# Kernel optimization log

Measured on AMD Instinct MI355X. Metric: run time of the kernel, lower is better.

Reference implementation:

```python
import jax, jax.numpy as jnp
import numpy as np

PRECS = 1e-05
# HBV parameter scaling bounds (order: BETA, FC, K0, K1, K2, LP, PERC, UZL, TT, CFMAX, CFR, CWH, BETAET)
LB = jnp.array([1.0, 50.0, 0.05, 0.01, 0.001, 0.2, 0.0, 0.0, -2.5, 0.5, 0.0, 0.0, 0.3], dtype=jnp.float32)
UB = jnp.array([6.0, 1000.0, 0.9, 0.5, 0.2, 1.0, 10.0, 100.0, 2.5, 10.0, 0.1, 0.2, 5.0], dtype=jnp.float32)

NSTEP, NGRID, MU = 730, 1000, 8

def setup_inputs() -> dict:
    key = jax.random.key(0)
    k1, k2, k3, k4 = jax.random.split(key, 4)
    P = jax.random.uniform(k1, (NSTEP, NGRID), jnp.float32) * 10.0      # precip mm/day
    T = jax.random.normal(k2, (NSTEP, NGRID), jnp.float32) * 8.0 + 2.0  # temp degC
    ET = jax.random.uniform(k3, (NSTEP, NGRID), jnp.float32) * 5.0      # PET mm/day
    x = jnp.stack([P, T, ET], axis=-1)                                   # [Nstep, Ngrid, 3]
    parameters = jax.random.uniform(k4, (NSTEP, NGRID, 13, MU), jnp.float32)  # raw in [0,1]
    tdlst = jnp.arange(2, dtype=jnp.int32)  # -> param indices {12, 0} = BETAET, BETA dynamic
    return {"x": x, "parameters": parameters, "staind": NSTEP - 1, "tdlst": tdlst, "mu": MU}

def _hbv_forward(x, parameters, staind, tdlst):
    # scale raw params to physical ranges: [Nstep, Ngrid, 13, mu]
    parT = LB[None, None, :, None] + parameters * (UB - LB)[None, None, :, None]
    # static params taken from time index staind, broadcast over time
    parhbv = jnp.broadcast_to(parT[staind][None], parT.shape)
    # dynamic params: dydrop=0 -> bernoulli mask is all zeros -> comPar = dynPar
    idx = jnp.mod(jnp.asarray(tdlst) - 1, 13)
    parhbv = parhbv.at[:, :, idx, :].set(parT[:, :, idx, :])

    Ngrid = x.shape[1]
    mu = parameters.shape[-1]
    init = tuple(jnp.full((Ngrid, mu), 0.001, dtype=jnp.float32) for _ in range(5))

    def step(carry, inp):
        SP, MW, SM, SUZ, SLZ = carry
        P_, T_, ET_, par = inp              # P_/T_/ET_: [Ngrid], par: [Ngrid, 13, mu]
        P_, T_, ET_ = P_[:, None], T_[:, None], ET_[:, None]
        BETA, FC, K0, K1, K2, LP, PERCc, UZL, TT, CFMAX, CFR, CWH, BETAET = (
            par[:, i] for i in range(13))
        is_rain = (T_ >= TT).astype(jnp.float32)
        RAIN = P_ * is_rain
        SNOW = P_ * (1.0 - is_rain)
        SP = SP + SNOW
        melt = jnp.minimum(jnp.maximum(CFMAX * (T_ - TT), 0.0), SP)
        MW = MW + melt
        SP = SP - melt
        refr = jnp.minimum(jnp.maximum(CFR * CFMAX * (TT - T_), 0.0), MW)
        SP = SP + refr
        MW = MW - refr
        tosoil = jnp.maximum(MW - CWH * SP, 0.0)
        MW = MW - tosoil
        soil_wetness = jnp.clip((SM / FC) ** BETA, 0.0, 1.0)
        recharge = (RAIN + tosoil) * soil_wetness
        SM = SM + RAIN + tosoil - recharge
        excess = jnp.maximum(SM - FC, 0.0)
        SM = SM - excess
        evapfactor = jnp.clip((SM / (LP * FC)) ** BETAET, 0.0, 1.0)
        ETact = jnp.minimum(SM, ET_ * evapfactor)
        SM = jnp.maximum(SM - ETact, PRECS)
        SUZ = SUZ + recharge + excess
        PERC = jnp.minimum(SUZ, PERCc)
        SUZ = SUZ - PERC
        Q0 = K0 * jnp.maximum(SUZ - UZL, 0.0)
        SUZ = SUZ - Q0
        Q1 = K1 * SUZ
        SUZ = SUZ - Q1
        SLZ = SLZ + PERC
        Q2 = K2 * SLZ
        SLZ = SLZ - Q2
        return (SP, MW, SM, SUZ, SLZ), Q0 + Q1 + Q2

    _, Qsimmu = jax.lax.scan(step, init, (x[:, :, 0], x[:, :, 1], x[:, :, 2], parhbv))
    # muwts=None -> mean over components; routOpt=False -> Qs = Qsimave[..., None]
    return Qsimmu.mean(-1)[..., None]  # [Nstep, Ngrid, 1]

def reference(x, parameters, staind, tdlst, mu):
    return _hbv_forward(x, parameters, staind, tdlst)
```

## Files before the change

kernel.cpp:

```cpp
#include <hip/hip_runtime.h>

#define NSTEP 730
#define NGRID 1000
#define MU    8
#define NPAR  13
#define PRECS 1e-5f

#define PAR_TSTRIDE 104000u
#define PAR_GSTRIDE 104u
#define X_TSTRIDE 3000u

#define GSTEPS 10
#define NGROUP (NSTEP / GSTEPS)

#define G5  5
#define NG5 (NSTEP / G5)

constexpr float LB_[NPAR] = {1.0f, 50.0f, 0.05f, 0.01f, 0.001f, 0.2f, 0.0f,
                             0.0f, -2.5f, 0.5f, 0.0f, 0.0f, 0.3f};
constexpr float UB_[NPAR] = {6.0f, 1000.0f, 0.9f, 0.5f, 0.2f, 1.0f, 10.0f,
                             100.0f, 2.5f, 10.0f, 0.1f, 0.2f, 5.0f};

__device__ __forceinline__ float fast_rcp(float x)  { return __builtin_amdgcn_rcpf(x); }
__device__ __forceinline__ float fast_exp2(float x) { return __builtin_amdgcn_exp2f(x); }
__device__ __forceinline__ float fast_log2(float x) { return __builtin_amdgcn_logf(x); }

__device__ __forceinline__ int mod13(int v) {
    int r = v % NPAR;
    if (r < 0) r += NPAR;
    return r;
}

template <int CTRL>
__device__ __forceinline__ float dpp_xadd(float v) {
    int r = __builtin_amdgcn_update_dpp(0, __float_as_int(v), CTRL, 0xF, 0xF, true);
    return v + __int_as_float(r);
}
__device__ __forceinline__ float mu8_sum(float v) {
    v = dpp_xadd<0xB1>(v);
    v = dpp_xadd<0x4E>(v);
    int s = __builtin_amdgcn_ds_swizzle(__float_as_int(v), 0x101F);
    return v + __int_as_float(s);
}

__device__ __forceinline__ void hbv_fast_12_0(
    const float* __restrict__ x, const float* __restrict__ par,
    int staind, float* __restrict__ out, int g, int m)
{
    const unsigned cpar = (unsigned)g * PAR_GSTRIDE + (unsigned)m;
    const unsigned g3   = (unsigned)g * 3u;

    float fx[NPAR];
    const unsigned sbase = (unsigned)staind * PAR_TSTRIDE + cpar;
#pragma unroll
    for (int i = 0; i < NPAR; ++i)
        fx[i] = fmaf(par[sbase + (unsigned)i * 8u], UB_[i] - LB_[i], LB_[i]);
    const float FC = fx[1], K0 = fx[2], K1 = fx[3], K2 = fx[4], LP = fx[5],
                PERCc = fx[6], UZL = fx[7], TT = fx[8], CFMAX = fx[9],
                CFR = fx[10], CWH = fx[11];
    const float rcpFC    = fast_rcp(FC);
    const float rcpLPFC  = fast_rcp(LP * FC);
    const float l2rcpFC  = fast_log2(rcpFC);
    const float l2rcpLPF = fast_log2(rcpLPFC);
    const float CC       = CFR * CFMAX;
    constexpr float lbB = LB_[0],  dvB = UB_[0]  - LB_[0];
    constexpr float lbE = LB_[12], dvE = UB_[12] - LB_[12];

    float bP[3][G5], bT[3][G5], bE[3][G5], b0[3][G5], b1[3][G5];
    float SP = 0.001f, MW = 0.001f, SM = 0.001f, SUZ = 0.001f, SLZ = 0.001f;

    auto load = [&](int b, int t0) {
#pragma unroll
        for (int j = 0; j < G5; ++j) {
            unsigned t  = (unsigned)(t0 + j);
            unsigned xo = t * X_TSTRIDE + g3;
            bP[b][j] = x[xo];
            bT[b][j] = x[xo + 1u];
            bE[b][j] = x[xo + 2u];
            unsigned po = t * PAR_TSTRIDE + cpar;
            b0[b][j] = par[po + 96u];
            b1[b][j] = par[po + 0u];
        }
    };

    auto compute = [&](int b, int t0) {
        float RAINv[G5], SNOWv[G5], MAXCM[G5], MAXRF[G5], ETv[G5];
        float BETAv[G5], BETEv[G5], bbc[G5], ebc[G5];
#pragma unroll
        for (int j = 0; j < G5; ++j) {
            float Pj = bP[b][j], Tj = bT[b][j];
            float dT = Tj - TT;
            float RAIN = (dT >= 0.f) ? Pj : 0.f;
            RAINv[j] = RAIN;
            SNOWv[j] = Pj - RAIN;
            float cm = CFMAX * dT;
            MAXCM[j] = fmaxf(cm, 0.f);
            MAXRF[j] = fmaxf(-CC * dT, 0.f);
            ETv[j]   = bE[b][j];
            float BETAET = fmaf(b0[b][j], dvE, lbE);
            float BETA   = fmaf(b1[b][j], dvB, lbB);
            BETAv[j] = BETA;  BETEv[j] = BETAET;
            bbc[j] = BETA   * l2rcpFC;
            ebc[j] = BETAET * l2rcpLPF;
        }
        float ql[G5];
#pragma unroll
        for (int j = 0; j < G5; ++j) {
            SP += SNOWv[j];
            float melt = fminf(MAXCM[j], SP);
            MW += melt; SP -= melt;
            float refr = fminf(MAXRF[j], MW);
            SP += refr; MW -= refr;
            float tosoil = fmaxf(fmaf(-CWH, SP, MW), 0.f);
            MW -= tosoil;
            float rt   = RAINv[j] + tosoil;
            float smrt = SM + rt;
            float soilw = fast_exp2(fmaf(BETAv[j], fast_log2(SM), bbc[j]));
            float rech  = rt * soilw;
            float SM_mid = smrt - rech;
            float SM_ae  = fminf(SM_mid, FC);
            float excess = SM_mid - SM_ae;
            float evapf  = fminf(fast_exp2(fmaf(BETEv[j], fast_log2(SM_ae), ebc[j])), 1.f);
            SM = fmaxf(fmaf(-ETv[j], evapf, SM_ae), PRECS);
            SUZ += rech + excess;
            float PERC = fminf(SUZ, PERCc);
            float SUZp = SUZ - PERC;
            float Q0   = K0 * fmaxf(SUZp - UZL, 0.f);
            float SUZq = SUZp - Q0;
            float Q1   = K1 * SUZq;
            SUZ = SUZq - Q1;
            SLZ += PERC;
            float Q2 = K2 * SLZ;
            SLZ -= Q2;
            ql[j] = (Q0 + Q1) + Q2;
        }
#pragma unroll
        for (int j = 0; j < G5; ++j) ql[j] = mu8_sum(ql[j]);
        if (m == 0) {
#pragma unroll
            for (int j = 0; j < G5; ++j)
                out[(unsigned)(t0 + j) * (unsigned)NGRID + (unsigned)g] = ql[j] * 0.125f;
        }
    };

    load(0, 0);
    load(1, G5);
    int grp = 0;
    for (int it = 0; it < 48; ++it, grp += 3) {
        load(2, (grp + 2) * G5); compute(0, grp * G5);
        load(0, (grp + 3) * G5); compute(1, (grp + 1) * G5);
        load(1, (grp + 4) * G5); compute(2, (grp + 2) * G5);
    }
    compute(0, 144 * G5);
    compute(1, 145 * G5);
}

__device__ __forceinline__ float hbv_step_core(
    float P_, float T_, float ET_,
    float BETA, float FC, float K0, float K1, float K2,
    float PERCc, float UZL, float TT, float CFMAX, float CFR, float CWH,
    float BETAET, float rcpFC, float rcpLPFC,
    float& SP, float& MW, float& SM, float& SUZ, float& SLZ)
{
    float dT    = T_ - TT;
    float RAIN  = (T_ >= TT) ? P_ : 0.f;
    float SNOW  = P_ - RAIN;
    SP += SNOW;
    float cm    = CFMAX * dT;
    float melt  = fminf(fmaxf(cm, 0.f), SP);
    MW += melt; SP -= melt;
    float refr  = fminf(fmaxf(-CFR * cm, 0.f), MW);
    SP += refr; MW -= refr;
    float tosoil = fmaxf(MW - CWH * SP, 0.f);
    MW -= tosoil;
    float soilw  = fminf(fast_exp2(BETA * fast_log2(SM * rcpFC)), 1.f);
    float rt     = RAIN + tosoil;
    float rech   = rt * soilw;
    SM += rt - rech;
    float excess = fmaxf(SM - FC, 0.f);
    SM -= excess;
    float evapf  = fminf(fast_exp2(BETAET * fast_log2(SM * rcpLPFC)), 1.f);
    float ETact  = fminf(SM, ET_ * evapf);
    SM = fmaxf(SM - ETact, PRECS);
    SUZ += rech + excess;
    float PERC = fminf(SUZ, PERCc);
    SUZ -= PERC;
    float Q0 = K0 * fmaxf(SUZ - UZL, 0.f);
    SUZ -= Q0;
    float Q1 = K1 * SUZ;
    SUZ -= Q1;
    SLZ += PERC;
    float Q2 = K2 * SLZ;
    SLZ -= Q2;
    return Q0 + Q1 + Q2;
}

__device__ void hbv_generic2(
    const float* __restrict__ x, const float* __restrict__ par,
    int staind, int idx0, int idx1, float* __restrict__ out, int g, int m)
{
    const unsigned cpar = (unsigned)g * PAR_GSTRIDE + (unsigned)m;
    const unsigned g3   = (unsigned)g * 3u;

    float lb0 = 0.f, dv0 = 0.f, lb1 = 0.f, dv1 = 0.f;
    float sel0[NPAR], sel1[NPAR];
#pragma unroll
    for (int i = 0; i < NPAR; ++i) {
        sel0[i] = (idx0 == i) ? 1.f : 0.f;
        sel1[i] = (idx1 == i && idx1 != idx0) ? 1.f : 0.f;
        if (idx0 == i) { lb0 = LB_[i]; dv0 = UB_[i] - LB_[i]; }
        if (idx1 == i) { lb1 = LB_[i]; dv1 = UB_[i] - LB_[i]; }
    }
    const unsigned off0 = (unsigned)idx0 * 8u, off1 = (unsigned)idx1 * 8u;

    float basep[NPAR];
    const unsigned sbase = (unsigned)staind * PAR_TSTRIDE + cpar;
#pragma unroll
    for (int i = 0; i < NPAR; ++i) {
        float fxv = fmaf(par[sbase + (unsigned)i * 8u], UB_[i] - LB_[i], LB_[i]);
        basep[i] = fxv * (1.f - sel0[i] - sel1[i]);
    }

    float bP[2][GSTEPS], bT[2][GSTEPS], bEv[2][GSTEPS];
    float bS0[2][GSTEPS], bS1[2][GSTEPS];
    float SP = 0.001f, MW = 0.001f, SM = 0.001f, SUZ = 0.001f, SLZ = 0.001f;

    auto load = [&](int b, int t0) {
#pragma unroll
        for (int j = 0; j < GSTEPS; ++j) {
            unsigned t  = (unsigned)(t0 + j);
            unsigned xo = t * X_TSTRIDE + g3;
            bP[b][j]  = x[xo];
            bT[b][j]  = x[xo + 1u];
            bEv[b][j] = x[xo + 2u];
            unsigned po = t * PAR_TSTRIDE + cpar;
            bS0[b][j] = par[po + off0];
            bS1[b][j] = par[po + off1];
        }
    };
    auto compute = [&](int b, int t0) {
        float ql[GSTEPS];
#pragma unroll
        for (int j = 0; j < GSTEPS; ++j) {
            float sv0 = fmaf(bS0[b][j], dv0, lb0);
            float sv1 = fmaf(bS1[b][j], dv1, lb1);
            float pr[NPAR];
#pragma unroll
            for (int i = 0; i < NPAR; ++i)
                pr[i] = fmaf(sel1[i], sv1, fmaf(sel0[i], sv0, basep[i]));
            float rcpFC   = fast_rcp(pr[1]);
            float rcpLPFC = fast_rcp(pr[5] * pr[1]);
            ql[j] = hbv_step_core(bP[b][j], bT[b][j], bEv[b][j],
                                  pr[0], pr[1], pr[2], pr[3], pr[4], pr[6],
                                  pr[7], pr[8], pr[9], pr[10], pr[11], pr[12],
                                  rcpFC, rcpLPFC, SP, MW, SM, SUZ, SLZ);
        }
#pragma unroll
        for (int j = 0; j < GSTEPS; ++j) {
            float s = mu8_sum(ql[j]);
            if (m == 0)
                out[(unsigned)(t0 + j) * (unsigned)NGRID + (unsigned)g] = s * 0.125f;
        }
    };

    load(0, 0);
    for (int gp = 0; gp < NGROUP; gp += 2) {
        if (gp + 1 < NGROUP) load(1, (gp + 1) * GSTEPS);
        compute(0, gp * GSTEPS);
        if (gp + 2 < NGROUP) load(0, (gp + 2) * GSTEPS);
        if (gp + 1 < NGROUP) compute(1, (gp + 1) * GSTEPS);
    }
}

__global__ __launch_bounds__(64, 1) void hbv_main(
    const float* __restrict__ x, const float* __restrict__ par,
    const int* __restrict__ staind_p, const int* __restrict__ tdlst_p,
    float* __restrict__ out)
{
    const int tid = blockIdx.x * 64 + threadIdx.x;
    const int g   = tid >> 3;
    const int m   = tid & 7;

    const int staind = __builtin_amdgcn_readfirstlane(staind_p[0]);
    const int idx0   = __builtin_amdgcn_readfirstlane(mod13(tdlst_p[0] - 1));
    const int idx1   = __builtin_amdgcn_readfirstlane(mod13(tdlst_p[1] - 1));

    if (idx0 == 12 && idx1 == 0)
        hbv_fast_12_0(x, par, staind, out, g, m);
    else
        hbv_generic2(x, par, staind, idx0, idx1, out, g, m);
}

__global__ __launch_bounds__(64, 1) void hbv_scan_generic(
    const float* __restrict__ x, const float* __restrict__ par,
    const int* __restrict__ staind_p, const int* __restrict__ tdlst_p,
    int n_td, float* __restrict__ out)
{
    const int tid = blockIdx.x * 64 + threadIdx.x;
    const int g   = tid >> 3;
    const int m   = tid & 7;
    if (g >= NGRID) return;

    const int staind    = staind_p[0];
    const unsigned cpar = (unsigned)g * PAR_GSTRIDE + (unsigned)m;
    const unsigned g3   = (unsigned)g * 3u;

    unsigned off[NPAR], st[NPAR];
#pragma unroll
    for (int i = 0; i < NPAR; ++i) {
        bool vr = false;
        for (int j = 0; j < n_td; ++j)
            if (mod13(tdlst_p[j] - 1) == i) vr = true;
        off[i] = (vr ? 0u : (unsigned)staind * PAR_TSTRIDE) + cpar + (unsigned)i * 8u;
        st[i]  = vr ? PAR_TSTRIDE : 0u;
    }

    float SP = 0.001f, MW = 0.001f, SM = 0.001f, SUZ = 0.001f, SLZ = 0.001f;
    for (int t = 0; t < NSTEP; ++t) {
        unsigned xo = (unsigned)t * X_TSTRIDE + g3;
        float P_ = x[xo], T_ = x[xo + 1u], E_ = x[xo + 2u];
        float pr[NPAR];
#pragma unroll
        for (int i = 0; i < NPAR; ++i) {
            pr[i] = fmaf(par[off[i]], UB_[i] - LB_[i], LB_[i]);
            off[i] += st[i];
        }
        float rcpFC   = fast_rcp(pr[1]);
        float rcpLPFC = fast_rcp(pr[5] * pr[1]);
        float q = hbv_step_core(P_, T_, E_, pr[0], pr[1], pr[2], pr[3], pr[4],
                                pr[6], pr[7], pr[8], pr[9], pr[10], pr[11],
                                pr[12], rcpFC, rcpLPFC, SP, MW, SM, SUZ, SLZ);
        float s = mu8_sum(q);
        if (m == 0) out[(unsigned)t * (unsigned)NGRID + (unsigned)g] = s * 0.125f;
    }
}

extern "C" void kernel_launch(void* const* d_in, const int* in_sizes, int n_in,
                              void* d_out, int out_size, void* d_ws, size_t ws_size,
                              hipStream_t stream) {
    const float* x      = (const float*)d_in[0];
    const float* par    = (const float*)d_in[1];
    const int*   staind = (const int*)d_in[2];
    const int*   tdlst  = (const int*)d_in[3];
    float*       out    = (float*)d_out;
    const int n_td = in_sizes[3];

    const int threads = NGRID * MU;
    const int block   = 64;
    const int grid    = (threads + block - 1) / block;

    if (n_td == 2)
        hbv_main<<<grid, block, 0, stream>>>(x, par, staind, tdlst, out);
    else
        hbv_scan_generic<<<grid, block, 0, stream>>>(x, par, staind, tdlst,
                                                     n_td, out);
}
```

Baseline: 430.9 us.

## Split HBV scan into producer and consumer waves with LDS double buffering

Each block now holds two waves. A producer wave loads forcing and dynamic parameters three groups ahead, precomputes the per-step terms (rain/snow split, melt limits, exponent constants) into double-buffered LDS, and reduces and writes the outputs. The consumer wave runs only the serial recurrence, reading precomputed inputs from LDS. The aim is to take global-memory latency, the preparation math and the reductions off the serial dependency chain. The cost is a __syncthreads per group of 10 steps plus extra LDS traffic, and the grid is still only 125 blocks.

Result: faster. 420.7 us (-2.4%).

```diff
diff --git a/kernel.cpp b/kernel.cpp
--- a/kernel.cpp
+++ b/kernel.cpp
@@ -2,7 +2,6 @@
 
 #define NSTEP 730
 #define NGRID 1000
-#define MU    8
 #define NPAR  13
 #define PRECS 1e-5f
 
@@ -10,11 +9,16 @@
 #define PAR_GSTRIDE 104u
 #define X_TSTRIDE 3000u
 
+#define G10   10
+#define NG10  73
+
 #define GSTEPS 10
-#define NGROUP (NSTEP / GSTEPS)
-
-#define G5  5
-#define NG5 (NSTEP / G5)
+#define NGROUP 73
+
+#define LDS_PREP_BUF 5760
+#define LDS_QL_BASE  11520
+#define LDS_QL_BUF   640
+#define LDS_TOTAL    12800
 
 constexpr float LB_[NPAR] = {1.0f, 50.0f, 0.05f, 0.01f, 0.001f, 0.2f, 0.0f,
                              0.0f, -2.5f, 0.5f, 0.0f, 0.0f, 0.3f};
@@ -41,118 +45,6 @@
     v = dpp_xadd<0x4E>(v);
     int s = __builtin_amdgcn_ds_swizzle(__float_as_int(v), 0x101F);
     return v + __int_as_float(s);
-}
-
-__device__ __forceinline__ void hbv_fast_12_0(
-    const float* __restrict__ x, const float* __restrict__ par,
-    int staind, float* __restrict__ out, int g, int m)
-{
-    const unsigned cpar = (unsigned)g * PAR_GSTRIDE + (unsigned)m;
-    const unsigned g3   = (unsigned)g * 3u;
-
-    float fx[NPAR];
-    const unsigned sbase = (unsigned)staind * PAR_TSTRIDE + cpar;
-#pragma unroll
-    for (int i = 0; i < NPAR; ++i)
-        fx[i] = fmaf(par[sbase + (unsigned)i * 8u], UB_[i] - LB_[i], LB_[i]);
-    const float FC = fx[1], K0 = fx[2], K1 = fx[3], K2 = fx[4], LP = fx[5],
-                PERCc = fx[6], UZL = fx[7], TT = fx[8], CFMAX = fx[9],
-                CFR = fx[10], CWH = fx[11];
-    const float rcpFC    = fast_rcp(FC);
-    const float rcpLPFC  = fast_rcp(LP * FC);
-    const float l2rcpFC  = fast_log2(rcpFC);
-    const float l2rcpLPF = fast_log2(rcpLPFC);
-    const float CC       = CFR * CFMAX;
-    constexpr float lbB = LB_[0],  dvB = UB_[0]  - LB_[0];
-    constexpr float lbE = LB_[12], dvE = UB_[12] - LB_[12];
-
-    float bP[3][G5], bT[3][G5], bE[3][G5], b0[3][G5], b1[3][G5];
-    float SP = 0.001f, MW = 0.001f, SM = 0.001f, SUZ = 0.001f, SLZ = 0.001f;
-
-    auto load = [&](int b, int t0) {
-#pragma unroll
-        for (int j = 0; j < G5; ++j) {
-            unsigned t  = (unsigned)(t0 + j);
-            unsigned xo = t * X_TSTRIDE + g3;
-            bP[b][j] = x[xo];
-            bT[b][j] = x[xo + 1u];
-            bE[b][j] = x[xo + 2u];
-            unsigned po = t * PAR_TSTRIDE + cpar;
-            b0[b][j] = par[po + 96u];
-            b1[b][j] = par[po + 0u];
-        }
-    };
-
-    auto compute = [&](int b, int t0) {
-        float RAINv[G5], SNOWv[G5], MAXCM[G5], MAXRF[G5], ETv[G5];
-        float BETAv[G5], BETEv[G5], bbc[G5], ebc[G5];
-#pragma unroll
-        for (int j = 0; j < G5; ++j) {
-            float Pj = bP[b][j], Tj = bT[b][j];
-            float dT = Tj - TT;
-            float RAIN = (dT >= 0.f) ? Pj : 0.f;
-            RAINv[j] = RAIN;
-            SNOWv[j] = Pj - RAIN;
-            float cm = CFMAX * dT;
-            MAXCM[j] = fmaxf(cm, 0.f);
-            MAXRF[j] = fmaxf(-CC * dT, 0.f);
-            ETv[j]   = bE[b][j];
-            float BETAET = fmaf(b0[b][j], dvE, lbE);
-            float BETA   = fmaf(b1[b][j], dvB, lbB);
-            BETAv[j] = BETA;  BETEv[j] = BETAET;
-            bbc[j] = BETA   * l2rcpFC;
-            ebc[j] = BETAET * l2rcpLPF;
-        }
-        float ql[G5];
-#pragma unroll
-        for (int j = 0; j < G5; ++j) {
-            SP += SNOWv[j];
-            float melt = fminf(MAXCM[j], SP);
-            MW += melt; SP -= melt;
-            float refr = fminf(MAXRF[j], MW);
-            SP += refr; MW -= refr;
-            float tosoil = fmaxf(fmaf(-CWH, SP, MW), 0.f);
-            MW -= tosoil;
-            float rt   = RAINv[j] + tosoil;
-            float smrt = SM + rt;
-            float soilw = fast_exp2(fmaf(BETAv[j], fast_log2(SM), bbc[j]));
-            float rech  = rt * soilw;
-            float SM_mid = smrt - rech;
-            float SM_ae  = fminf(SM_mid, FC);
-            float excess = SM_mid - SM_ae;
-            float evapf  = fminf(fast_exp2(fmaf(BETEv[j], fast_log2(SM_ae), ebc[j])), 1.f);
-            SM = fmaxf(fmaf(-ETv[j], evapf, SM_ae), PRECS);
-            SUZ += rech + excess;
-            float PERC = fminf(SUZ, PERCc);
-            float SUZp = SUZ - PERC;
-            float Q0   = K0 * fmaxf(SUZp - UZL, 0.f);
-            float SUZq = SUZp - Q0;
-            float Q1   = K1 * SUZq;
-            SUZ = SUZq - Q1;
-            SLZ += PERC;
-            float Q2 = K2 * SLZ;
-            SLZ -= Q2;
-            ql[j] = (Q0 + Q1) + Q2;
-        }
-#pragma unroll
-        for (int j = 0; j < G5; ++j) ql[j] = mu8_sum(ql[j]);
-        if (m == 0) {
-#pragma unroll
-            for (int j = 0; j < G5; ++j)
-                out[(unsigned)(t0 + j) * (unsigned)NGRID + (unsigned)g] = ql[j] * 0.125f;
-        }
-    };
-
-    load(0, 0);
-    load(1, G5);
-    int grp = 0;
-    for (int it = 0; it < 48; ++it, grp += 3) {
-        load(2, (grp + 2) * G5); compute(0, grp * G5);
-        load(0, (grp + 3) * G5); compute(1, (grp + 1) * G5);
-        load(1, (grp + 4) * G5); compute(2, (grp + 2) * G5);
-    }
-    compute(0, 144 * G5);
-    compute(1, 145 * G5);
 }
 
 __device__ __forceinline__ float hbv_step_core(
@@ -272,23 +164,166 @@
     }
 }
 
-__global__ __launch_bounds__(64, 1) void hbv_main(
+__global__ __launch_bounds__(128, 1) void hbv_pc(
     const float* __restrict__ x, const float* __restrict__ par,
     const int* __restrict__ staind_p, const int* __restrict__ tdlst_p,
     float* __restrict__ out)
 {
-    const int tid = blockIdx.x * 64 + threadIdx.x;
-    const int g   = tid >> 3;
-    const int m   = tid & 7;
+    __shared__ float lds[LDS_TOTAL];
+
+    const int lane  = threadIdx.x & 63;
+    const int wave  = threadIdx.x >> 6;
+    const int chain = blockIdx.x * 64 + lane;
+    const int g = chain >> 3;
+    const int m = chain & 7;
 
     const int staind = __builtin_amdgcn_readfirstlane(staind_p[0]);
     const int idx0   = __builtin_amdgcn_readfirstlane(mod13(tdlst_p[0] - 1));
     const int idx1   = __builtin_amdgcn_readfirstlane(mod13(tdlst_p[1] - 1));
 
-    if (idx0 == 12 && idx1 == 0)
-        hbv_fast_12_0(x, par, staind, out, g, m);
-    else
-        hbv_generic2(x, par, staind, idx0, idx1, out, g, m);
+    if (!(idx0 == 12 && idx1 == 0)) {
+        if (wave == 0) hbv_generic2(x, par, staind, idx0, idx1, out, g, m);
+        return;
+    }
+
+    const unsigned cpar = (unsigned)g * PAR_GSTRIDE + (unsigned)m;
+    const unsigned g3   = (unsigned)g * 3u;
+
+    float fx[NPAR];
+    const unsigned sbase = (unsigned)staind * PAR_TSTRIDE + cpar;
+#pragma unroll
+    for (int i = 0; i < NPAR; ++i)
+        fx[i] = fmaf(par[sbase + (unsigned)i * 8u], UB_[i] - LB_[i], LB_[i]);
+
+    if (wave == 0) {
+        const float TT = fx[8], CFMAX = fx[9], CC = fx[10] * fx[9];
+        const float rcpFC    = fast_rcp(fx[1]);
+        const float rcpLPFC  = fast_rcp(fx[5] * fx[1]);
+        const float l2rcpFC  = fast_log2(rcpFC);
+        const float l2rcpLPF = fast_log2(rcpLPFC);
+        constexpr float lbB = LB_[0],  dvB = UB_[0]  - LB_[0];
+        constexpr float lbE = LB_[12], dvE = UB_[12] - LB_[12];
+
+        float vP[3][G10], vT[3][G10], vE[3][G10], v0[3][G10], v1[3][G10];
+
+        auto gload = [&](int b, int grp) {
+            int t0 = grp * G10;
+#pragma unroll
+            for (int j = 0; j < G10; ++j) {
+                unsigned t  = (unsigned)(t0 + j);
+                unsigned xo = t * X_TSTRIDE + g3;
+                vP[b][j] = x[xo];
+                vT[b][j] = x[xo + 1u];
+                vE[b][j] = x[xo + 2u];
+                unsigned po = t * PAR_TSTRIDE + cpar;
+                v0[b][j] = par[po + 96u];
+                v1[b][j] = par[po];
+            }
+        };
+        auto prep = [&](int b, int dbuf) {
+            float* pw = &lds[dbuf * LDS_PREP_BUF + lane];
+#pragma unroll
+            for (int j = 0; j < G10; ++j) {
+                float Pj = vP[b][j], Tj = vT[b][j];
+                float dT   = Tj - TT;
+                float RAIN = (dT >= 0.f) ? Pj : 0.f;
+                float BETAET = fmaf(v0[b][j], dvE, lbE);
+                float BETA   = fmaf(v1[b][j], dvB, lbB);
+                pw[(j * 9 + 0) * 64] = Pj - RAIN;
+                pw[(j * 9 + 1) * 64] = fmaxf(CFMAX * dT, 0.f);
+                pw[(j * 9 + 2) * 64] = fmaxf(-CC * dT, 0.f);
+                pw[(j * 9 + 3) * 64] = RAIN;
+                pw[(j * 9 + 4) * 64] = vE[b][j];
+                pw[(j * 9 + 5) * 64] = BETA * l2rcpFC;
+                pw[(j * 9 + 6) * 64] = BETAET * l2rcpLPF;
+                pw[(j * 9 + 7) * 64] = BETA;
+                pw[(j * 9 + 8) * 64] = BETAET;
+            }
+        };
+        auto red = [&](int sbuf, int grp) {
+            const float* qb = &lds[LDS_QL_BASE + sbuf * LDS_QL_BUF + lane];
+            float s[G10];
+#pragma unroll
+            for (int j = 0; j < G10; ++j) s[j] = mu8_sum(qb[j * 64]);
+            if (m == 0) {
+#pragma unroll
+                for (int j = 0; j < G10; ++j)
+                    out[(unsigned)(grp * G10 + j) * (unsigned)NGRID + (unsigned)g]
+                        = s[j] * 0.125f;
+            }
+        };
+
+#define PHASE(kk, BL, BP)                                   \
+        {                                                   \
+            __syncthreads();                                \
+            if ((kk) + 3 < NG10) gload(BL, (kk) + 3);       \
+            if ((kk) + 1 < NG10) prep(BP, ((kk) + 1) & 1);  \
+            if ((kk) >= 1) red(((kk) - 1) & 1, (kk) - 1);   \
+        }
+
+        gload(0, 0); gload(1, 1); gload(2, 2);
+        prep(0, 0);
+        int k = 0;
+        for (int t = 0; t < 24; ++t) {
+            PHASE(k, 0, 1); ++k;
+            PHASE(k, 1, 2); ++k;
+            PHASE(k, 2, 0); ++k;
+        }
+        PHASE(k, 0, 1);
+        __syncthreads();
+        red(0, 72);
+#undef PHASE
+    } else {
+        const float FC = fx[1], K0 = fx[2], K1 = fx[3], K2 = fx[4],
+                    PERCc = fx[6], UZL = fx[7], CWH = fx[11];
+        float SP = 0.001f, MW = 0.001f, SM = 0.001f, SUZ = 0.001f, SLZ = 0.001f;
+
+        for (int k = 0; k < NG10; ++k) {
+            __syncthreads();
+            const float* pr = &lds[(k & 1) * LDS_PREP_BUF + lane];
+            float* qw = &lds[LDS_QL_BASE + (k & 1) * LDS_QL_BUF + lane];
+#pragma unroll
+            for (int j = 0; j < G10; ++j) {
+                float SNOW   = pr[(j * 9 + 0) * 64];
+                float MAXCM  = pr[(j * 9 + 1) * 64];
+                float MAXRF  = pr[(j * 9 + 2) * 64];
+                float RAIN   = pr[(j * 9 + 3) * 64];
+                float ET     = pr[(j * 9 + 4) * 64];
+                float bbc    = pr[(j * 9 + 5) * 64];
+                float ebc    = pr[(j * 9 + 6) * 64];
+                float BETA   = pr[(j * 9 + 7) * 64];
+                float BETAET = pr[(j * 9 + 8) * 64];
+
+                SP += SNOW;
+                float melt = fminf(MAXCM, SP);
+                MW += melt; SP -= melt;
+                float refr = fminf(MAXRF, MW);
+                SP += refr; MW -= refr;
+                float tosoil = fmaxf(fmaf(-CWH, SP, MW), 0.f);
+                MW -= tosoil;
+                float rt    = RAIN + tosoil;
+                float soilw = fast_exp2(fmaf(BETA, fast_log2(SM), bbc));
+                float rech  = rt * soilw;
+                float SM_mid = SM + rt - rech;
+                float SM_ae  = fminf(SM_mid, FC);
+                float excess = SM_mid - SM_ae;
+                float evapf  = fminf(fast_exp2(fmaf(BETAET, fast_log2(SM_ae), ebc)), 1.f);
+                SM = fmaxf(fmaf(-ET, evapf, SM_ae), PRECS);
+                SUZ += rech + excess;
+                float PERC = fminf(SUZ, PERCc);
+                float SUZp = SUZ - PERC;
+                float Q0   = K0 * fmaxf(SUZp - UZL, 0.f);
+                float SUZq = SUZp - Q0;
+                float Q1   = K1 * SUZq;
+                SUZ = SUZq - Q1;
+                SLZ += PERC;
+                float Q2 = K2 * SLZ;
+                SLZ -= Q2;
+                qw[j * 64] = (Q0 + Q1) + Q2;
+            }
+        }
+        __syncthreads();
+    }
 }
 
 __global__ __launch_bounds__(64, 1) void hbv_scan_generic(
@@ -345,13 +380,10 @@
     float*       out    = (float*)d_out;
     const int n_td = in_sizes[3];
 
-    const int threads = NGRID * MU;
-    const int block   = 64;
-    const int grid    = (threads + block - 1) / block;
-
-    if (n_td == 2)
-        hbv_main<<<grid, block, 0, stream>>>(x, par, staind, tdlst, out);
-    else
-        hbv_scan_generic<<<grid, block, 0, stream>>>(x, par, staind, tdlst,
-                                                     n_td, out);
-}
+    if (n_td == 2) {
+        hbv_pc<<<125, 128, 0, stream>>>(x, par, staind, tdlst, out);
+    } else {
+        hbv_scan_generic<<<125, 64, 0, stream>>>(x, par, staind, tdlst,
+                                                 n_td, out);
+    }
+}
```
